# Kernel optimization log

Measured on AMD Instinct MI355X. Metric: run time of the kernel, lower is better.

The kernel has to match this reference:

```python
import jax, jax.numpy as jnp
import numpy as np

N = 100000      # nodes
E = 1200000     # edges
H = 64          # hidden_channels
L = 8           # num_layers
G = 100         # graphs in batch
ALPHA = 0.1
THETA = 0.5
EPS = 1e-5      # BatchNorm1d eps


def setup_inputs() -> dict:
    key = jax.random.key(0)
    ks = jax.random.split(key, 12)
    s = 0.05
    pos = jax.random.normal(ks[0], (N, 3), dtype=jnp.float32)
    edge_index = jax.random.randint(ks[1], (2, E), 0, N, dtype=jnp.int32)
    batch = jnp.sort(jax.random.randint(ks[2], (N,), 0, G, dtype=jnp.int32))
    return {
        "pos": pos,
        "edge_index": edge_index,
        "batch": batch,
        "lin0_w": jax.random.normal(ks[3], (3, H), dtype=jnp.float32) * s,
        "lin0_b": jnp.zeros((H,), jnp.float32),
        "conv_w": jax.random.normal(ks[4], (L, H, H), dtype=jnp.float32) * s,
        "lin1_w": jax.random.normal(ks[5], (H, H), dtype=jnp.float32) * s,
        "lin1_b": jnp.zeros((H,), jnp.float32),
        "mlp1_w": jax.random.normal(ks[6], (H, H), dtype=jnp.float32) * s,
        "mlp1_b": jnp.zeros((H,), jnp.float32),
        "bn1_g": jnp.ones((H,), jnp.float32),
        "bn1_b": jnp.zeros((H,), jnp.float32),
        "mlp2_w": jax.random.normal(ks[7], (H, H), dtype=jnp.float32) * s,
        "mlp2_b": jnp.zeros((H,), jnp.float32),
        "bn2_g": jnp.ones((H,), jnp.float32),
        "bn2_b": jnp.zeros((H,), jnp.float32),
        "out_w": jax.random.normal(ks[8], (H, 10), dtype=jnp.float32) * s,
        "out_b": jnp.zeros((10,), jnp.float32),
    }


def _bn(z, g, b):
    # BatchNorm1d, training-mode batch statistics
    mu = z.mean(axis=0)
    var = z.var(axis=0)
    return g * (z - mu) * jax.lax.rsqrt(var + EPS) + b


def reference(pos, edge_index, batch, lin0_w, lin0_b, conv_w, lin1_w, lin1_b,
              mlp1_w, mlp1_b, bn1_g, bn1_b, mlp2_w, mlp2_b, bn2_g, bn2_b,
              out_w, out_b):
    src, dst = edge_index[0], edge_index[1]
    x = jax.nn.relu(pos @ lin0_w + lin0_b)   # [N, H]
    x0 = x
    for l in range(L):
        beta = float(np.log(THETA / (l + 1) + 1.0))
        # GCN2Conv (normalize=False, shared_weights=True):
        # sum-aggregate neighbors, initial residual, identity mapping
        agg = jax.ops.segment_sum(x[src], dst, num_segments=N)   # [N, H]
        h = (1.0 - ALPHA) * agg + ALPHA * x0
        x = jax.nn.relu((1.0 - beta) * h + beta * (h @ conv_w[l]))
    x = x @ lin1_w + lin1_b
    pooled = jax.ops.segment_max(x, batch, num_segments=G)       # [G, H]
    pooled = jnp.where(jnp.isfinite(pooled), pooled, 0.0)        # guard empty segments
    h1 = jax.nn.relu(_bn(pooled @ mlp1_w + mlp1_b, bn1_g, bn1_b))
    h2 = jax.nn.relu(_bn(h1 @ mlp2_w + mlp2_b, bn2_g, bn2_b))
    logits = h2 @ out_w + out_b                                  # [G, 10]
    return jax.nn.log_softmax(logits, axis=-1)
```

## Files before the change

kernel.cpp:

```cpp
#include <hip/hip_runtime.h>
#include <hip/hip_fp16.h>
#include <math.h>

#define NNODES 100000
#define NEDGES 1200000
#define HD 64
#define NLAYERS 8
#define NGRAPH 100
#define PPART 32
#define C8 16777216.0f

__device__ __forceinline__ float h2f(__half h) { return __half2float(h); }
__device__ __forceinline__ __half f2h(float f) { return __float2half(f); }

__global__ void lin0_k(const float* __restrict__ pos, const float* __restrict__ w,
                       const float* __restrict__ b, float* __restrict__ x0f,
                       __half* __restrict__ x0h, int total) {
    int i = blockIdx.x * blockDim.x + threadIdx.x;
    if (i >= total) return;
    int n = i >> 6, h = i & 63;
    float p0 = pos[n * 3 + 0], p1 = pos[n * 3 + 1], p2 = pos[n * 3 + 2];
    float v = fmaf(p0, w[h], fmaf(p1, w[64 + h], fmaf(p2, w[128 + h], b[h])));
    v = fmaxf(v, 0.0f);
    x0f[i] = v;
    x0h[i] = f2h(v);
}

__global__ void hist_k(const int* __restrict__ dst, int* __restrict__ deg,
                       int* __restrict__ rank, int E) {
    int e = blockIdx.x * blockDim.x + threadIdx.x;
    if (e < E) rank[e] = atomicAdd(&deg[dst[e]], 1);
}

__global__ void scan_part_k(const int* __restrict__ deg, int* __restrict__ bsum, int n) {
    __shared__ int s[256];
    int t = threadIdx.x;
    int i = blockIdx.x * 256 + t;
    s[t] = (i < n) ? deg[i] : 0;
    __syncthreads();
    for (int off = 128; off > 0; off >>= 1) {
        if (t < off) s[t] += s[t + off];
        __syncthreads();
    }
    if (t == 0) bsum[blockIdx.x] = s[0];
}

__global__ void scan_mid_k(const int* __restrict__ bsum, int* __restrict__ boff,
                           int nblk, int* __restrict__ roff, int n) {
    __shared__ int s[512];
    int t = threadIdx.x;
    int v = (t < nblk) ? bsum[t] : 0;
    s[t] = v;
    __syncthreads();
    for (int off = 1; off < 512; off <<= 1) {
        int u = (t >= off) ? s[t - off] : 0;
        __syncthreads();
        s[t] += u;
        __syncthreads();
    }
    if (t < nblk) boff[t] = s[t] - v;
    if (t == nblk - 1) roff[n] = s[t];
}

__global__ void scan_final_k(const int* __restrict__ deg, const int* __restrict__ boff,
                             int* __restrict__ roff, int n) {
    __shared__ int s[256];
    int t = threadIdx.x;
    int i = blockIdx.x * 256 + t;
    int v = (i < n) ? deg[i] : 0;
    s[t] = v;
    __syncthreads();
    for (int off = 1; off < 256; off <<= 1) {
        int u = (t >= off) ? s[t - off] : 0;
        __syncthreads();
        s[t] += u;
        __syncthreads();
    }
    if (i < n) roff[i] = boff[blockIdx.x] + s[t] - v;
}

__global__ void fill_k(const int* __restrict__ src, const int* __restrict__ dst,
                       const int* __restrict__ roff, const int* __restrict__ rank,
                       int* __restrict__ csr, int E) {
    int e = blockIdx.x * blockDim.x + threadIdx.x;
    if (e < E) csr[roff[dst[e]] + rank[e]] = src[e];
}

__global__ __launch_bounds__(256, 8) void layer_k(
    const __half* __restrict__ xin, __half* __restrict__ xout,
    const float* __restrict__ x0, const float* __restrict__ W,
    const int* __restrict__ roff, const int* __restrict__ csr,
    float beta, float x0scale, int total_waves) {
    __shared__ __align__(16) float MT[64 * 64];
    __shared__ __align__(16) float hrow[4][64];
    const int tid   = threadIdx.x;
    const int lane  = tid & 63;
    const int wslot = tid >> 6;
    const float omb = 1.0f - beta;
    for (int idx = tid; idx < 4096; idx += 256) {
        int k = idx >> 6, j = idx & 63;
        float m = beta * W[idx];
        if (k == j) m += omb;
        m *= 0.125f;
        MT[j * 64 + (((k >> 2) ^ (j & 15)) << 2) + (k & 3)] = m;
    }
    __syncthreads();
    const int wid0 = (blockIdx.x * blockDim.x + tid) >> 6;
    for (int n = wid0; n < NNODES; n += total_waves) {
        const int beg = roff[n], end = roff[n + 1];
        float x0v = x0[(n << 6) + lane];
        float s0 = 0.0f, s1 = 0.0f, s2 = 0.0f, s3 = 0.0f;
        int i = beg;
        for (; i + 8 <= end; i += 8) {
            int e0 = csr[i + 0], e1 = csr[i + 1], e2 = csr[i + 2], e3 = csr[i + 3];
            int e4 = csr[i + 4], e5 = csr[i + 5], e6 = csr[i + 6], e7 = csr[i + 7];
            __half a0 = xin[(e0 << 6) + lane];
            __half a1 = xin[(e1 << 6) + lane];
            __half a2 = xin[(e2 << 6) + lane];
            __half a3 = xin[(e3 << 6) + lane];
            __half a4 = xin[(e4 << 6) + lane];
            __half a5 = xin[(e5 << 6) + lane];
            __half a6 = xin[(e6 << 6) + lane];
            __half a7 = xin[(e7 << 6) + lane];
            s0 += h2f(a0); s1 += h2f(a1); s2 += h2f(a2); s3 += h2f(a3);
            s0 += h2f(a4); s1 += h2f(a5); s2 += h2f(a6); s3 += h2f(a7);
        }
        for (; i + 4 <= end; i += 4) {
            int e0 = csr[i + 0], e1 = csr[i + 1], e2 = csr[i + 2], e3 = csr[i + 3];
            s0 += h2f(xin[(e0 << 6) + lane]);
            s1 += h2f(xin[(e1 << 6) + lane]);
            s2 += h2f(xin[(e2 << 6) + lane]);
            s3 += h2f(xin[(e3 << 6) + lane]);
        }
        for (; i < end; ++i) s0 += h2f(xin[(csr[i] << 6) + lane]);
        float agg = (s0 + s1) + (s2 + s3);
        float h = fmaf(0.9f, agg, x0scale * x0v);
        hrow[wslot][lane] = h;
        __builtin_amdgcn_wave_barrier();
        float a0 = 0.0f, a1 = 0.0f, a2 = 0.0f, a3 = 0.0f;
#pragma unroll
        for (int g = 0; g < 16; ++g) {
            float4 hv = *(const float4*)&hrow[wslot][g * 4];
            float4 mv = *(const float4*)&MT[(lane << 6) + ((g ^ (lane & 15)) << 2)];
            a0 = fmaf(hv.x, mv.x, a0);
            a1 = fmaf(hv.y, mv.y, a1);
            a2 = fmaf(hv.z, mv.z, a2);
            a3 = fmaf(hv.w, mv.w, a3);
        }
        __builtin_amdgcn_wave_barrier();
        float o = (a0 + a1) + (a2 + a3);
        xout[(n << 6) + lane] = f2h(fmaxf(o, 0.0f));
    }
}

__device__ __forceinline__ int lbound(const int* __restrict__ a, int n, int v) {
    int lo = 0, hi = n;
    while (lo < hi) { int mid = (lo + hi) >> 1; if (a[mid] < v) lo = mid + 1; else hi = mid; }
    return lo;
}

__global__ __launch_bounds__(256, 8) void poolpart_k(
    const __half* __restrict__ xin, const float* __restrict__ W,
    const float* __restrict__ bvec, const int* __restrict__ batch,
    float* __restrict__ pmax) {
    __shared__ __align__(16) float MT[64 * 64];
    __shared__ __align__(16) float hrow[4][64];
    __shared__ float wm[4][64];
    const int tid   = threadIdx.x;
    const int lane  = tid & 63;
    const int wslot = tid >> 6;
    for (int idx = tid; idx < 4096; idx += 256) {
        int k = idx >> 6, j = idx & 63;
        MT[j * 64 + (((k >> 2) ^ (j & 15)) << 2) + (k & 3)] = W[idx];
    }
    __syncthreads();
    const int g = blockIdx.x / PPART, part = blockIdx.x % PPART;
    const int lo = lbound(batch, NNODES, g);
    const int hi = lbound(batch, NNODES, g + 1);
    const int cnt = hi - lo;
    const int qlo = lo + (cnt * part) / PPART;
    const int qhi = lo + (cnt * (part + 1)) / PPART;
    const float bias = bvec[lane];
    float vmax = -INFINITY;
    for (int n = qlo + wslot; n < qhi; n += 4) {
        hrow[wslot][lane] = h2f(xin[(n << 6) + lane]);
        __builtin_amdgcn_wave_barrier();
        float a0 = 0.0f, a1 = 0.0f, a2 = 0.0f, a3 = 0.0f;
#pragma unroll
        for (int gg = 0; gg < 16; ++gg) {
            float4 hv = *(const float4*)&hrow[wslot][gg * 4];
            float4 mv = *(const float4*)&MT[(lane << 6) + ((gg ^ (lane & 15)) << 2)];
            a0 = fmaf(hv.x, mv.x, a0);
            a1 = fmaf(hv.y, mv.y, a1);
            a2 = fmaf(hv.z, mv.z, a2);
            a3 = fmaf(hv.w, mv.w, a3);
        }
        __builtin_amdgcn_wave_barrier();
        float acc = (a0 + a1) + (a2 + a3);
        vmax = fmaxf(vmax, fmaf(C8, acc, bias));
    }
    wm[wslot][lane] = vmax;
    __syncthreads();
    if (tid < 64) {
        float m = fmaxf(fmaxf(wm[0][tid], wm[1][tid]), fmaxf(wm[2][tid], wm[3][tid]));
        pmax[blockIdx.x * 64 + tid] = m;
    }
}

__global__ void poolcomb_k(const float* __restrict__ pmax, float* __restrict__ pooled) {
    int i = blockIdx.x * blockDim.x + threadIdx.x;
    if (i >= NGRAPH * 64) return;
    int g = i >> 6, lane = i & 63;
    float m = -INFINITY;
    for (int p = 0; p < PPART; ++p)
        m = fmaxf(m, pmax[(PPART * g + p) * 64 + lane]);
    pooled[i] = m;
}

__global__ __launch_bounds__(256) void head_k(
    const float* __restrict__ pooled,
    const float* __restrict__ m1w, const float* __restrict__ m1b,
    const float* __restrict__ g1, const float* __restrict__ be1,
    const float* __restrict__ m2w, const float* __restrict__ m2b,
    const float* __restrict__ g2, const float* __restrict__ be2,
    const float* __restrict__ ow, const float* __restrict__ ob,
    float* __restrict__ out) {
    __shared__ float A[NGRAPH * 64];
    __shared__ float B[NGRAPH * 64];
    __shared__ float mu[64], rs[64];
    __shared__ float LG[NGRAPH * 10];
    int t = threadIdx.x;
    for (int i = t; i < NGRAPH * 64; i += 256) {
        float f = pooled[i];
        if (!isfinite(f)) f = 0.0f;
        A[i] = f;
    }
    __syncthreads();
    for (int i = t; i < NGRAPH * 64; i += 256) {
        int g = i >> 6, j = i & 63;
        float acc = m1b[j];
        for (int k = 0; k < 64; ++k) acc = fmaf(A[(g << 6) + k], m1w[k * 64 + j], acc);
        B[i] = acc;
    }
    __syncthreads();
    if (t < 64) {
        float sm = 0.0f, sq = 0.0f;
        for (int g = 0; g < NGRAPH; ++g) { float z = B[g * 64 + t]; sm += z; sq += z * z; }
        float m = sm * (1.0f / NGRAPH);
        float var = sq * (1.0f / NGRAPH) - m * m;
        mu[t] = m; rs[t] = rsqrtf(var + 1e-5f);
    }
    __syncthreads();
    for (int i = t; i < NGRAPH * 64; i += 256) {
        int j = i & 63;
        float z = fmaf((B[i] - mu[j]) * rs[j], g1[j], be1[j]);
        A[i] = fmaxf(z, 0.0f);
    }
    __syncthreads();
    for (int i = t; i < NGRAPH * 64; i += 256) {
        int g = i >> 6, j = i & 63;
        float acc = m2b[j];
        for (int k = 0; k < 64; ++k) acc = fmaf(A[(g << 6) + k], m2w[k * 64 + j], acc);
        B[i] = acc;
    }
    __syncthreads();
    if (t < 64) {
        float sm = 0.0f, sq = 0.0f;
        for (int g = 0; g < NGRAPH; ++g) { float z = B[g * 64 + t]; sm += z; sq += z * z; }
        float m = sm * (1.0f / NGRAPH);
        float var = sq * (1.0f / NGRAPH) - m * m;
        mu[t] = m; rs[t] = rsqrtf(var + 1e-5f);
    }
    __syncthreads();
    for (int i = t; i < NGRAPH * 64; i += 256) {
        int j = i & 63;
        float z = fmaf((B[i] - mu[j]) * rs[j], g2[j], be2[j]);
        A[i] = fmaxf(z, 0.0f);
    }
    __syncthreads();
    for (int i = t; i < NGRAPH * 10; i += 256) {
        int g = i / 10, j = i - g * 10;
        float acc = ob[j];
        for (int k = 0; k < 64; ++k) acc = fmaf(A[(g << 6) + k], ow[k * 10 + j], acc);
        LG[i] = acc;
    }
    __syncthreads();
    if (t < NGRAPH) {
        float m = -1e30f;
        for (int j = 0; j < 10; ++j) m = fmaxf(m, LG[t * 10 + j]);
        float s = 0.0f;
        for (int j = 0; j < 10; ++j) s += expf(LG[t * 10 + j] - m);
        float lse = m + logf(s);
        for (int j = 0; j < 10; ++j) out[t * 10 + j] = LG[t * 10 + j] - lse;
    }
}

extern "C" void kernel_launch(void* const* d_in, const int* in_sizes, int n_in,
                              void* d_out, int out_size, void* d_ws, size_t ws_size,
                              hipStream_t stream) {
    const float* pos   = (const float*)d_in[0];
    const int*   eidx  = (const int*)d_in[1];
    const int*   batch = (const int*)d_in[2];
    const float* l0w   = (const float*)d_in[3];
    const float* l0b   = (const float*)d_in[4];
    const float* cw    = (const float*)d_in[5];
    const float* l1w   = (const float*)d_in[6];
    const float* l1b   = (const float*)d_in[7];
    const float* m1w   = (const float*)d_in[8];
    const float* m1b   = (const float*)d_in[9];
    const float* g1    = (const float*)d_in[10];
    const float* b1    = (const float*)d_in[11];
    const float* m2w   = (const float*)d_in[12];
    const float* m2b   = (const float*)d_in[13];
    const float* g2    = (const float*)d_in[14];
    const float* b2    = (const float*)d_in[15];
    const float* ow    = (const float*)d_in[16];
    const float* ob    = (const float*)d_in[17];
    float* out = (float*)d_out;
    const int* src = eidx;
    const int* dst = eidx + NEDGES;

    size_t off = 0;
    auto alloc = [&](size_t bytes) -> void* {
        void* p = (char*)d_ws + off;
        off += (bytes + 255) & ~(size_t)255;
        return p;
    };
    float*  x0f    = (float*)alloc((size_t)NNODES * 64 * 4);
    __half* x0h    = (__half*)alloc((size_t)NNODES * 64 * 2);
    __half* xA     = (__half*)alloc((size_t)NNODES * 64 * 2);
    __half* xB     = (__half*)alloc((size_t)NNODES * 64 * 2);
    int*    deg    = (int*)alloc((size_t)NNODES * 4);
    int*    roff   = (int*)alloc((size_t)(NNODES + 1) * 4);
    const int NBLK = (NNODES + 255) / 256;
    int*    bsum   = (int*)alloc((size_t)NBLK * 4);
    int*    boff   = (int*)alloc((size_t)NBLK * 4);
    int*    csr    = (int*)alloc((size_t)NEDGES * 4);
    float*  pooled = (float*)alloc((size_t)NGRAPH * 64 * 4);
    float*  pmax   = (float*)alloc((size_t)NGRAPH * PPART * 64 * 4);
    int*    rank   = (int*)xB;

    hipMemsetAsync(deg, 0, (size_t)NNODES * 4, stream);
    {
        int total = NNODES * 64;
        lin0_k<<<(total + 255) / 256, 256, 0, stream>>>(pos, l0w, l0b, x0f, x0h, total);
    }
    hist_k<<<(NEDGES + 255) / 256, 256, 0, stream>>>(dst, deg, rank, NEDGES);
    scan_part_k<<<NBLK, 256, 0, stream>>>(deg, bsum, NNODES);
    scan_mid_k<<<1, 512, 0, stream>>>(bsum, boff, NBLK, roff, NNODES);
    scan_final_k<<<NBLK, 256, 0, stream>>>(deg, boff, roff, NNODES);
    fill_k<<<(NEDGES + 255) / 256, 256, 0, stream>>>(src, dst, roff, rank, csr, NEDGES);

    const int LBLOCKS = 2048;
    const int TW = LBLOCKS * 256 / 64;
    const __half* cur = x0h;
    for (int l = 0; l < NLAYERS; ++l) {
        float beta    = (float)log(0.5 / (double)(l + 1) + 1.0);
        float x0scale = (float)(0.1 * ldexp(1.0, -3 * l));
        __half* nxt = (l & 1) ? xB : xA;
        layer_k<<<LBLOCKS, 256, 0, stream>>>(cur, nxt, x0f, cw + (size_t)l * 4096,
                                             roff, csr, beta, x0scale, TW);
        cur = nxt;
    }
    poolpart_k<<<NGRAPH * PPART, 256, 0, stream>>>(cur, l1w, l1b, batch, pmax);
    poolcomb_k<<<(NGRAPH * 64 + 255) / 256, 256, 0, stream>>>(pmax, pooled);
    head_k<<<1, 256, 0, stream>>>(pooled, m1w, m1b, g1, b1, m2w, m2b, g2, b2, ow, ob, out);
}
```

Measured before the change: 620.9 us.

## Process four nodes per wave with readlane broadcast in layer matvec

Each wave now handles a group of four nodes. It gathers the four aggregated rows into registers, then does the 64x64 transform with readlane broadcasts instead of staging each row through shared memory. Each MT float4 load from LDS is reused across four nodes, and the per-node LDS writes and wave barriers go away. The cost is four times fewer independent work items per wave and serialized gathers per group. The four gathers may also issue fewer concurrent loads if the compiler does not interleave them.

```diff
diff --git a/kernel.cpp b/kernel.cpp
--- a/kernel.cpp
+++ b/kernel.cpp
@@ -12,6 +12,10 @@
 
 __device__ __forceinline__ float h2f(__half h) { return __half2float(h); }
 __device__ __forceinline__ __half f2h(float f) { return __float2half(f); }
+
+__device__ __forceinline__ float rl(float v, int l) {
+    return __uint_as_float(__builtin_amdgcn_readlane(__float_as_uint(v), l));
+}
 
 __global__ void lin0_k(const float* __restrict__ pos, const float* __restrict__ w,
                        const float* __restrict__ b, float* __restrict__ x0f,
@@ -86,16 +90,52 @@
     if (e < E) csr[roff[dst[e]] + rank[e]] = src[e];
 }
 
+#define GATHER(hb, nn)                                                          \
+    {                                                                           \
+        const int nu  = (nn);                                                   \
+        const int beg = roff[nu], end = roff[nu + 1];                           \
+        float x0v = x0[(nu << 6) + lane];                                       \
+        float s0 = 0.0f, s1 = 0.0f, s2 = 0.0f, s3 = 0.0f;                       \
+        int i = beg;                                                            \
+        for (; i + 8 <= end; i += 8) {                                          \
+            int e0 = csr[i + 0], e1 = csr[i + 1], e2 = csr[i + 2], e3 = csr[i + 3]; \
+            int e4 = csr[i + 4], e5 = csr[i + 5], e6 = csr[i + 6], e7 = csr[i + 7]; \
+            __half b0 = xin[(e0 << 6) + lane];                                  \
+            __half b1 = xin[(e1 << 6) + lane];                                  \
+            __half b2 = xin[(e2 << 6) + lane];                                  \
+            __half b3 = xin[(e3 << 6) + lane];                                  \
+            __half b4 = xin[(e4 << 6) + lane];                                  \
+            __half b5 = xin[(e5 << 6) + lane];                                  \
+            __half b6 = xin[(e6 << 6) + lane];                                  \
+            __half b7 = xin[(e7 << 6) + lane];                                  \
+            s0 += h2f(b0); s1 += h2f(b1); s2 += h2f(b2); s3 += h2f(b3);         \
+            s0 += h2f(b4); s1 += h2f(b5); s2 += h2f(b6); s3 += h2f(b7);         \
+        }                                                                       \
+        for (; i + 4 <= end; i += 4) {                                          \
+            int e0 = csr[i + 0], e1 = csr[i + 1], e2 = csr[i + 2], e3 = csr[i + 3]; \
+            s0 += h2f(xin[(e0 << 6) + lane]);                                   \
+            s1 += h2f(xin[(e1 << 6) + lane]);                                   \
+            s2 += h2f(xin[(e2 << 6) + lane]);                                   \
+            s3 += h2f(xin[(e3 << 6) + lane]);                                   \
+        }                                                                       \
+        for (; i < end; ++i) s0 += h2f(xin[(csr[i] << 6) + lane]);              \
+        hb = fmaf(0.9f, (s0 + s1) + (s2 + s3), x0scale * x0v);                  \
+    }
+
+#define MLPSTEP(kk, comp)                                                       \
+    a0 = fmaf(rl(h0, kk), mv.comp, a0);                                         \
+    a1 = fmaf(rl(h1, kk), mv.comp, a1);                                         \
+    a2 = fmaf(rl(h2, kk), mv.comp, a2);                                         \
+    a3 = fmaf(rl(h3, kk), mv.comp, a3);
+
 __global__ __launch_bounds__(256, 8) void layer_k(
     const __half* __restrict__ xin, __half* __restrict__ xout,
     const float* __restrict__ x0, const float* __restrict__ W,
     const int* __restrict__ roff, const int* __restrict__ csr,
     float beta, float x0scale, int total_waves) {
     __shared__ __align__(16) float MT[64 * 64];
-    __shared__ __align__(16) float hrow[4][64];
-    const int tid   = threadIdx.x;
-    const int lane  = tid & 63;
-    const int wslot = tid >> 6;
+    const int tid  = threadIdx.x;
+    const int lane = tid & 63;
     const float omb = 1.0f - beta;
     for (int idx = tid; idx < 4096; idx += 256) {
         int k = idx >> 6, j = idx & 63;
@@ -106,50 +146,26 @@
     }
     __syncthreads();
     const int wid0 = (blockIdx.x * blockDim.x + tid) >> 6;
-    for (int n = wid0; n < NNODES; n += total_waves) {
-        const int beg = roff[n], end = roff[n + 1];
-        float x0v = x0[(n << 6) + lane];
-        float s0 = 0.0f, s1 = 0.0f, s2 = 0.0f, s3 = 0.0f;
-        int i = beg;
-        for (; i + 8 <= end; i += 8) {
-            int e0 = csr[i + 0], e1 = csr[i + 1], e2 = csr[i + 2], e3 = csr[i + 3];
-            int e4 = csr[i + 4], e5 = csr[i + 5], e6 = csr[i + 6], e7 = csr[i + 7];
-            __half a0 = xin[(e0 << 6) + lane];
-            __half a1 = xin[(e1 << 6) + lane];
-            __half a2 = xin[(e2 << 6) + lane];
-            __half a3 = xin[(e3 << 6) + lane];
-            __half a4 = xin[(e4 << 6) + lane];
-            __half a5 = xin[(e5 << 6) + lane];
-            __half a6 = xin[(e6 << 6) + lane];
-            __half a7 = xin[(e7 << 6) + lane];
-            s0 += h2f(a0); s1 += h2f(a1); s2 += h2f(a2); s3 += h2f(a3);
-            s0 += h2f(a4); s1 += h2f(a5); s2 += h2f(a6); s3 += h2f(a7);
-        }
-        for (; i + 4 <= end; i += 4) {
-            int e0 = csr[i + 0], e1 = csr[i + 1], e2 = csr[i + 2], e3 = csr[i + 3];
-            s0 += h2f(xin[(e0 << 6) + lane]);
-            s1 += h2f(xin[(e1 << 6) + lane]);
-            s2 += h2f(xin[(e2 << 6) + lane]);
-            s3 += h2f(xin[(e3 << 6) + lane]);
-        }
-        for (; i < end; ++i) s0 += h2f(xin[(csr[i] << 6) + lane]);
-        float agg = (s0 + s1) + (s2 + s3);
-        float h = fmaf(0.9f, agg, x0scale * x0v);
-        hrow[wslot][lane] = h;
-        __builtin_amdgcn_wave_barrier();
+    for (int grp = wid0; grp < NNODES / 4; grp += total_waves) {
+        const int nb = grp << 2;
+        float h0, h1, h2, h3;
+        GATHER(h0, nb + 0)
+        GATHER(h1, nb + 1)
+        GATHER(h2, nb + 2)
+        GATHER(h3, nb + 3)
         float a0 = 0.0f, a1 = 0.0f, a2 = 0.0f, a3 = 0.0f;
 #pragma unroll
         for (int g = 0; g < 16; ++g) {
-            float4 hv = *(const float4*)&hrow[wslot][g * 4];
             float4 mv = *(const float4*)&MT[(lane << 6) + ((g ^ (lane & 15)) << 2)];
-            a0 = fmaf(hv.x, mv.x, a0);
-            a1 = fmaf(hv.y, mv.y, a1);
-            a2 = fmaf(hv.z, mv.z, a2);
-            a3 = fmaf(hv.w, mv.w, a3);
+            MLPSTEP(4 * g + 0, x)
+            MLPSTEP(4 * g + 1, y)
+            MLPSTEP(4 * g + 2, z)
+            MLPSTEP(4 * g + 3, w)
         }
-        __builtin_amdgcn_wave_barrier();
-        float o = (a0 + a1) + (a2 + a3);
-        xout[(n << 6) + lane] = f2h(fmaxf(o, 0.0f));
+        xout[((nb + 0) << 6) + lane] = f2h(fmaxf(a0, 0.0f));
+        xout[((nb + 1) << 6) + lane] = f2h(fmaxf(a1, 0.0f));
+        xout[((nb + 2) << 6) + lane] = f2h(fmaxf(a2, 0.0f));
+        xout[((nb + 3) << 6) + lane] = f2h(fmaxf(a3, 0.0f));
     }
 }
 
```

After: 974.7 us. 1.57x slower.
